# Kernel tuning notes

Hardware: AMD Instinct MI355X
Metric: run time of the kernel (lower is better)

## Reference

```python
import jax, jax.numpy as jnp
import numpy as np

H = 512  # hidden_size
L = 2    # num_layers


def setup_inputs() -> dict:
    key = jax.random.key(0)
    ks = jax.random.split(key, 10)
    B, S, I = 64, 512, 512
    s = 1.0 / np.sqrt(H)
    def w(k, shape):
        return jax.random.uniform(k, shape, jnp.float32, -s, s)
    return {
        "x": jax.random.normal(ks[0], (B, S, I), jnp.float32),
        "encoder_h": jax.random.normal(ks[1], (B, 2 * H), jnp.float32),
        "Wih_f": w(ks[2], (L, 3 * H, I)),
        "Whh_f": w(ks[3], (L, 3 * H, H)),
        "bih_f": w(ks[4], (L, 3 * H)),
        "bhh_f": w(ks[5], (L, 3 * H)),
        "Wih_b": w(ks[6], (L, 3 * H, I)),
        "Whh_b": w(ks[7], (L, 3 * H, H)),
        "bih_b": w(ks[8], (L, 3 * H)),
        "bhh_b": w(ks[9], (L, 3 * H)),
    }


def _run_direction(seq, h0, Wih, Whh, bih, bhh):
    """Stacked GRU over time. seq: [B,S,I], h0: [B,H]. Returns ([B,S,H], [B,H]).
    Equivalent to the per-timestep stacked-layer loop in the torch module: each
    layer consumes the previous layer's output stream and its own previous hidden."""
    h_last = h0
    for j in range(L):
        # Precompute input-side gates for the whole sequence (one big GEMM).
        gi = jnp.einsum('bsi,gi->bsg', seq, Wih[j]) + bih[j]  # [B,S,3H]
        Whh_j, bhh_j = Whh[j], bhh[j]

        def step(h, gi_t):
            gh = h @ Whh_j.T + bhh_j                 # [B,3H]
            i_r, i_z, i_n = jnp.split(gi_t, 3, axis=-1)
            h_r, h_z, h_n = jnp.split(gh, 3, axis=-1)
            r = jax.nn.sigmoid(i_r + h_r)
            z = jax.nn.sigmoid(i_z + h_z)
            n = jnp.tanh(i_n + r * h_n)
            h_new = (1.0 - z) * n + z * h
            return h_new, h_new

        h_last, outs = jax.lax.scan(step, h0, jnp.swapaxes(gi, 0, 1))  # outs: [S,B,H]
        seq = jnp.swapaxes(outs, 0, 1)  # [B,S,H] feeds next layer
    return seq, h_last


def reference(x, encoder_h, Wih_f, Whh_f, bih_f, bhh_f, Wih_b, Whh_b, bih_b, bhh_b):
    h0_f = encoder_h[:, :H]
    h0_b = encoder_h[:, H:]
    out_f, h_f = _run_direction(x, h0_f, Wih_f, Whh_f, bih_f, bhh_f)
    x_rev = jnp.flip(x, axis=1)
    out_b_rev, h_b = _run_direction(x_rev, h0_b, Wih_b, Whh_b, bih_b, bhh_b)
    out_b = jnp.flip(out_b_rev, axis=1)
    out = jnp.concatenate([out_f, out_b], axis=2)   # [B,S,2H]
    h = jnp.concatenate([h_f, h_b], axis=1)         # [B,2H]
    return out, h
```

## Files before the change

### kernel.cpp

```cpp
#include <hip/hip_runtime.h>


#define B_ 64
#define S_ 512
#define H_ 512
#define G3_ 1536

typedef __attribute__((ext_vector_type(8))) __bf16 bf16x8;
typedef __attribute__((ext_vector_type(8))) short short8;
typedef __attribute__((ext_vector_type(2))) unsigned long long ull2;
typedef __attribute__((ext_vector_type(4))) float f32x4;
typedef unsigned long long ull;

__device__ __forceinline__ unsigned short f2b(float f) {
  union { float f; unsigned int i; } v; v.f = f;
  unsigned int x = v.i;
  return (unsigned short)((x + 0x7fffu + ((x >> 16) & 1u)) >> 16);
}
__device__ __forceinline__ bf16x8 load8(const unsigned short* p) {
  short8 s = *(const short8*)p;
  return __builtin_bit_cast(bf16x8, s);
}
__device__ __forceinline__ bf16x8 load8f(const float* p) {
  f32x4 a = *(const f32x4*)p, b = *(const f32x4*)(p + 4);
  short8 s;
  s[0] = (short)f2b(a[0]); s[1] = (short)f2b(a[1]);
  s[2] = (short)f2b(a[2]); s[3] = (short)f2b(a[3]);
  s[4] = (short)f2b(b[0]); s[5] = (short)f2b(b[1]);
  s[6] = (short)f2b(b[2]); s[7] = (short)f2b(b[3]);
  return __builtin_bit_cast(bf16x8, s);
}
__device__ __forceinline__ f32x4 mfma16(bf16x8 a, bf16x8 b, f32x4 c) {
  return __builtin_amdgcn_mfma_f32_16x16x32_bf16(a, b, c, 0, 0, 0);
}
__device__ __forceinline__ float sigmoidf_(float x) {
  float e = __expf(-fabsf(x));
  float s = e / (1.0f + e);
  return x >= 0.0f ? 1.0f - s : s;
}
__device__ __forceinline__ float tanhf_(float x) {
  float e = __expf(-2.0f * fabsf(x));
  float r = (1.0f - e) / (1.0f + e);
  return x >= 0.0f ? r : -r;
}
__device__ __forceinline__ bf16x8 load16p(const ull* p) {
  ull2 v = *(const ull2*)p;
  return __builtin_bit_cast(bf16x8, v);
}
__device__ __forceinline__ bf16x8 ld16bypass(const ull* p) {
  short8 r;
  asm volatile("global_load_dwordx4 %0, %1, off sc0 sc1"
               : "=v"(r) : "v"(p) : "memory");
  return __builtin_bit_cast(bf16x8, r);
}

__global__ void cvt_x(const float* __restrict__ x, ull* __restrict__ xc) {
  int i = blockIdx.x * 256 + threadIdx.x;
  int b = i & 63, cell = (i >> 6) & 63, txx = i >> 12;
  const float* src = x + ((size_t)b * 512 + txx) * 512 + cell * 8;
  ull v0 = 0, v1 = 0;
#pragma unroll
  for (int j = 0; j < 4; ++j) v0 |= (ull)f2b(src[j]) << (16 * j);
#pragma unroll
  for (int j = 0; j < 4; ++j) v1 |= (ull)f2b(src[4 + j]) << (16 * j);
  size_t o = ((size_t)txx * 4096 + cell * 64 + b) * 2;
  xc[o] = v0;
  xc[o + 1] = v1;
}

__global__ void init_ring(const float* __restrict__ enc, ull* __restrict__ ring) {
  int i = blockIdx.x * 256 + threadIdx.x;
  if (i >= 32768) return;
  int gid = i >> 12;
  int u = i & 4095;
  int d = (gid >> 1) & 1, beta = gid & 1;
  int half = u & 1, b = (u >> 1) & 31, cell = u >> 6;
  const float* e = enc + (size_t)(beta * 32 + b) * 1024 + d * 512 + cell * 8 + half * 4;
  ull v = 0;
#pragma unroll
  for (int j = 0; j < 4; ++j) v |= (ull)f2b(e[j]) << (16 * j);
  ring[(size_t)gid * 32768 + 7 * 4096 + u] = v;
}

__global__ __launch_bounds__(128) void gru_fused(
    const float* __restrict__ x,
    const ull* __restrict__ xc, int usexc,
    const float* __restrict__ enc,
    const float* __restrict__ WihF, const float* __restrict__ WihB,
    const float* __restrict__ WhhF, const float* __restrict__ WhhB,
    const float* __restrict__ bihF, const float* __restrict__ bihB,
    const float* __restrict__ bhhF, const float* __restrict__ bhhB,
    ull* __restrict__ ring,
    unsigned int* __restrict__ flags,
    float* __restrict__ dout) {
  __shared__ __align__(16) unsigned short wih2[24576];
  __shared__ __align__(16) unsigned short whh2[24576];
  __shared__ float hpub[32 * 20];
  __shared__ __align__(16) float douts[8][32][20];
  __shared__ int lcnt[8];

  const int tid = threadIdx.x;
  const int lane = tid & 63;
  const int wv = tid >> 6;
  const int wg = (int)blockIdx.x;
  const int l = wg >> 7, d = (wg >> 6) & 1, beta = (wg >> 5) & 1, cb = wg & 31;
  const int gid = ((l * 2 + d) << 1) | beta;
  const int gidA = gid & 3;
  const int gidB = gidA | 4;
  const int colbase = cb * 16;
  const int rowA = lane & 15, kb = lane >> 4;

  const float* Wih = (d ? WihB : WihF) + (size_t)l * G3_ * H_;
  const float* Whh = (d ? WhhB : WhhF) + (size_t)l * G3_ * H_;
  const float* bi = (d ? bihB : bihF) + l * G3_;
  const float* bh = (d ? bhhB : bhhF) + l * G3_;

  if (tid < 8) lcnt[tid] = 0;
  for (int i = tid; i < 3072; i += 128) {
    int gate = i >> 10;
    int rest = i & 1023;
    int kk = rest >> 6;
    int l6 = rest & 63;
    int c = l6 & 15, k = l6 >> 4;
    size_t gro = (size_t)(gate * 512 + colbase + c) * 512 + kk * 32 + k * 8;
    *(short8*)&wih2[i * 8] = __builtin_bit_cast(short8, load8f(Wih + gro));
    *(short8*)&whh2[i * 8] = __builtin_bit_cast(short8, load8f(Whh + gro));
  }
  __syncthreads();

  const int col16 = rowA;
  const int hc = colbase + col16;
  const float brz_r = bi[hc] + bh[hc];
  const float brz_z = bi[512 + hc] + bh[512 + hc];
  const float bi_n = bi[1024 + hc];
  const float bh_n = bh[1024 + hc];

  const int bq = wv * 16 + kb * 4;
  const int arow = wv * 16 + rowA;

  float hm[4];
#pragma unroll
  for (int rg = 0; rg < 4; ++rg)
    hm[rg] = enc[(size_t)(beta * 32 + bq + rg) * 1024 + d * 512 + hc];

  unsigned int* flA = flags + gidA * 1024;
  unsigned int* flB = flags + gidB * 1024;
  unsigned int* flo = flags + gid * 1024;
  ull* ringA = ring + (size_t)gidA * 32768;
  ull* ringl = ring + (size_t)gid * 32768;

  const int pb = tid >> 2;
  const int pq = tid & 3;
  const int pcellL = pq >> 1, phalf = pq & 1;
  const int pidx = ((2 * cb + pcellL) * 32 + pb) * 2 + phalf;
  const int pc0 = pcellL * 8 + phalf * 4;

  for (int t = 0; t < 512; ++t) {
    bf16x8 aIn[16];
    if (l == 0) {
      int txx = d ? (511 - t) : t;
      if (usexc) {
        const ull* xp = xc + (size_t)txx * 8192;
#pragma unroll
        for (int kk = 0; kk < 16; ++kk)
          aIn[kk] = load16p(xp + (size_t)((kk * 4 + kb) * 64 + beta * 32 + arow) * 2);
      } else {
        const float* ap = x + ((size_t)(beta * 32 + arow) * 512 + txx) * 512 + kb * 8;
#pragma unroll
        for (int kk = 0; kk < 16; ++kk) aIn[kk] = load8f(ap + kk * 32);
      }
    }

    {
      const int needA = (l == 0) ? t : (t + 1);
      const int needB = (l == 0) ? (t - 7) : t;
      unsigned int* watch;
      int need;
      if (lane < 32) { watch = flA + lane * 32;        need = needA; }
      else           { watch = flB + (lane - 32) * 32; need = needB; }
      if (need > 0) {
        while (__hip_atomic_load(watch, __ATOMIC_RELAXED,
                                 __HIP_MEMORY_SCOPE_AGENT) < (unsigned)need) {}
      }
    }
    asm volatile("" ::: "memory");

    bf16x8 aOwn[16];
    ull* rpo = ringl + (size_t)((t + 7) & 7) * 4096;
#pragma unroll
    for (int kk = 0; kk < 16; ++kk)
      aOwn[kk] = ld16bypass(rpo + (size_t)((kk * 4 + kb) * 32 + arow) * 2);
    if (l == 1) {
      ull* rp = ringA + (size_t)(t & 7) * 4096;
#pragma unroll
      for (int kk = 0; kk < 16; ++kk)
        aIn[kk] = ld16bypass(rp + (size_t)((kk * 4 + kb) * 32 + arow) * 2);
    }
    asm volatile("s_waitcnt vmcnt(0)" ::: "memory");
    __builtin_amdgcn_sched_barrier(0);

    f32x4 accr = {0,0,0,0}, accz = {0,0,0,0}, acni = {0,0,0,0}, acnh = {0,0,0,0};
#pragma unroll
    for (int kk = 0; kk < 16; ++kk) {
      const int o = kk * 512 + lane * 8;
      accr = mfma16(aIn[kk],  load8(&wih2[o]), accr);
      accr = mfma16(aOwn[kk], load8(&whh2[o]), accr);
      accz = mfma16(aIn[kk],  load8(&wih2[8192 + o]), accz);
      accz = mfma16(aOwn[kk], load8(&whh2[8192 + o]), accz);
      acni = mfma16(aIn[kk],  load8(&wih2[16384 + o]), acni);
      acnh = mfma16(aOwn[kk], load8(&whh2[16384 + o]), acnh);
    }

#pragma unroll
    for (int rg = 0; rg < 4; ++rg) {
      float r = sigmoidf_(accr[rg] + brz_r);
      float z = sigmoidf_(accz[rg] + brz_z);
      float n = tanhf_(acni[rg] + bi_n + r * (acnh[rg] + bh_n));
      float hnew = (1.0f - z) * n + z * hm[rg];
      hm[rg] = hnew;
      hpub[(bq + rg) * 20 + col16] = hnew;
      if (l == 1) douts[t & 7][bq + rg][col16] = hnew;
    }
    asm volatile("" ::: "memory");

    {
      f32x4 v4 = *(f32x4*)&hpub[pb * 20 + pc0];
      ull v = 0;
      v |= (ull)f2b(v4[0]);
      v |= (ull)f2b(v4[1]) << 16;
      v |= (ull)f2b(v4[2]) << 32;
      v |= (ull)f2b(v4[3]) << 48;
      __hip_atomic_store(ringl + (size_t)(t & 7) * 4096 + pidx, v,
                         __ATOMIC_RELAXED, __HIP_MEMORY_SCOPE_AGENT);
    }
    asm volatile("s_waitcnt vmcnt(0)" ::: "memory");

    if (lane == 0) {
      int old = atomicAdd(&lcnt[t & 7], 1);
      if (old == 1) {
        lcnt[t & 7] = 0;
        __hip_atomic_store(flo + cb * 32, (unsigned)(t + 1),
                           __ATOMIC_RELAXED, __HIP_MEMORY_SCOPE_AGENT);
      }
    }

    if (l == 1 && (t & 7) == 7) {
      const int fb = tid >> 2;
      const int fc = (tid & 3) * 4;
#pragma unroll
      for (int ts = 0; ts < 8; ++ts) {
        int tt = t - 7 + ts;
        int tox = d ? (511 - tt) : tt;
        f32x4 v = *(f32x4*)&douts[ts][fb][fc];
        *(f32x4*)&dout[((size_t)(beta * 32 + fb) * 512 + tox) * 1024 +
                       d * 512 + colbase + fc] = v;
      }
    }
  }
}

__global__ void h_epi(float* __restrict__ dout) {
  int i = blockIdx.x * 256 + threadIdx.x;
  if (i >= B_ * 2 * H_) return;
  int b = i >> 10, j = i & 1023;
  int t = (j < H_) ? (S_ - 1) : 0;
  dout[(size_t)B_ * S_ * 2 * H_ + i] = dout[((size_t)b * S_ + t) * (2 * H_) + j];
}

extern "C" void kernel_launch(void* const* d_in, const int* in_sizes, int n_in,
                              void* d_out, int out_size, void* d_ws, size_t ws_size,
                              hipStream_t stream) {
  const float* x    = (const float*)d_in[0];
  const float* enc  = (const float*)d_in[1];
  const float* WihF = (const float*)d_in[2];
  const float* WhhF = (const float*)d_in[3];
  const float* bihF = (const float*)d_in[4];
  const float* bhhF = (const float*)d_in[5];
  const float* WihB = (const float*)d_in[6];
  const float* WhhB = (const float*)d_in[7];
  const float* bihB = (const float*)d_in[8];
  const float* bhhB = (const float*)d_in[9];
  float* out = (float*)d_out;

  char* ws = (char*)d_ws;
  unsigned int* flags = (unsigned int*)ws;
  ull* ring  = (ull*)(ws + 65536);
  ull* xc    = (ull*)(ws + 65536 + 2097152);
  const int usexc = (ws_size >= (size_t)65536 + 2097152 + 33554432) ? 1 : 0;

  (void)hipMemsetAsync(flags, 0, 32768, stream);
  if (usexc) cvt_x<<<8192, 256, 0, stream>>>(x, xc);
  init_ring<<<128, 256, 0, stream>>>(enc, ring);
  gru_fused<<<256, 128, 0, stream>>>(x, xc, usexc, enc,
                                     WihF, WihB, WhhF, WhhB,
                                     bihF, bihB, bhhF, bhhB,
                                     ring, flags, out);
  h_epi<<<256, 256, 0, stream>>>(out);
}
```

Before: 2.442 ms.

## Process both batch halves per workgroup, halving grid and interleaving steps

Each workgroup now handles both 32-row batch halves, looping over them inside each timestep, so the grid drops from 256 to 128 blocks. LDS-resident weights are shared across the two halves, and the work on one half can overlap the wait on the other half's flags. Ring loads switch from inline-asm cache-bypass loads to relaxed agent-scope atomic loads, and the explicit wait and sched barrier before the MFMAs are removed. The cost is serialized per-block work and half the CUs in use, which lengthens the per-step critical path.

```diff
diff --git a/kernel.cpp b/kernel.cpp
--- a/kernel.cpp
+++ b/kernel.cpp
@@ -43,15 +43,15 @@
   float r = (1.0f - e) / (1.0f + e);
   return x >= 0.0f ? r : -r;
 }
+__device__ __forceinline__ bf16x8 load16a(ull* p) {
+  ull2 v;
+  v[0] = __hip_atomic_load(p, __ATOMIC_RELAXED, __HIP_MEMORY_SCOPE_AGENT);
+  v[1] = __hip_atomic_load(p + 1, __ATOMIC_RELAXED, __HIP_MEMORY_SCOPE_AGENT);
+  return __builtin_bit_cast(bf16x8, v);
+}
 __device__ __forceinline__ bf16x8 load16p(const ull* p) {
   ull2 v = *(const ull2*)p;
   return __builtin_bit_cast(bf16x8, v);
-}
-__device__ __forceinline__ bf16x8 ld16bypass(const ull* p) {
-  short8 r;
-  asm volatile("global_load_dwordx4 %0, %1, off sc0 sc1"
-               : "=v"(r) : "v"(p) : "memory");
-  return __builtin_bit_cast(bf16x8, r);
 }
 
 __global__ void cvt_x(const float* __restrict__ x, ull* __restrict__ xc) {
@@ -95,18 +95,15 @@
     float* __restrict__ dout) {
   __shared__ __align__(16) unsigned short wih2[24576];
   __shared__ __align__(16) unsigned short whh2[24576];
-  __shared__ float hpub[32 * 20];
-  __shared__ __align__(16) float douts[8][32][20];
-  __shared__ int lcnt[8];
+  __shared__ float hpub[2][32 * 20];
+  __shared__ __align__(16) float douts[2][8][32][20];
+  __shared__ int lcnt[2][8];
 
   const int tid = threadIdx.x;
   const int lane = tid & 63;
   const int wv = tid >> 6;
   const int wg = (int)blockIdx.x;
-  const int l = wg >> 7, d = (wg >> 6) & 1, beta = (wg >> 5) & 1, cb = wg & 31;
-  const int gid = ((l * 2 + d) << 1) | beta;
-  const int gidA = gid & 3;
-  const int gidB = gidA | 4;
+  const int l = wg >> 6, d = (wg >> 5) & 1, cb = wg & 31;
   const int colbase = cb * 16;
   const int rowA = lane & 15, kb = lane >> 4;
 
@@ -115,7 +112,7 @@
   const float* bi = (d ? bihB : bihF) + l * G3_;
   const float* bh = (d ? bhhB : bhhF) + l * G3_;
 
-  if (tid < 8) lcnt[tid] = 0;
+  if (tid < 16) lcnt[tid >> 3][tid & 7] = 0;
   for (int i = tid; i < 3072; i += 128) {
     int gate = i >> 10;
     int rest = i & 1023;
@@ -138,16 +135,14 @@
   const int bq = wv * 16 + kb * 4;
   const int arow = wv * 16 + rowA;
 
-  float hm[4];
-#pragma unroll
-  for (int rg = 0; rg < 4; ++rg)
-    hm[rg] = enc[(size_t)(beta * 32 + bq + rg) * 1024 + d * 512 + hc];
-
-  unsigned int* flA = flags + gidA * 1024;
-  unsigned int* flB = flags + gidB * 1024;
-  unsigned int* flo = flags + gid * 1024;
-  ull* ringA = ring + (size_t)gidA * 32768;
-  ull* ringl = ring + (size_t)gid * 32768;
+  float hm[2][4];
+#pragma unroll
+  for (int be = 0; be < 2; ++be)
+#pragma unroll
+    for (int rg = 0; rg < 4; ++rg)
+      hm[be][rg] = enc[(size_t)(be * 32 + bq + rg) * 1024 + d * 512 + hc];
+
+  const int gidbase = (l * 2 + d) << 1;
 
   const int pb = tid >> 2;
   const int pq = tid & 3;
@@ -156,104 +151,112 @@
   const int pc0 = pcellL * 8 + phalf * 4;
 
   for (int t = 0; t < 512; ++t) {
-    bf16x8 aIn[16];
-    if (l == 0) {
-      int txx = d ? (511 - t) : t;
-      if (usexc) {
-        const ull* xp = xc + (size_t)txx * 8192;
+#pragma unroll
+    for (int be = 0; be < 2; ++be) {
+      const int gid = gidbase | be;
+      unsigned int* flA = flags + (gid & 3) * 1024;
+      unsigned int* flB = flags + ((gid & 3) | 4) * 1024;
+      unsigned int* flo = flags + gid * 1024;
+      ull* ringA = ring + (size_t)(gid & 3) * 32768;
+      ull* ringl = ring + (size_t)gid * 32768;
+
+      bf16x8 aIn[16];
+      if (l == 0) {
+        int txx = d ? (511 - t) : t;
+        if (usexc) {
+          const ull* xp = xc + (size_t)txx * 8192;
+#pragma unroll
+          for (int kk = 0; kk < 16; ++kk)
+            aIn[kk] = load16p(xp + (size_t)((kk * 4 + kb) * 64 + be * 32 + arow) * 2);
+        } else {
+          const float* ap = x + ((size_t)(be * 32 + arow) * 512 + txx) * 512 + kb * 8;
+#pragma unroll
+          for (int kk = 0; kk < 16; ++kk) aIn[kk] = load8f(ap + kk * 32);
+        }
+      }
+
+      {
+        const int needA = (l == 0) ? t : (t + 1);
+        const int needB = (l == 0) ? (t - 7) : t;
+        unsigned int* watch;
+        int need;
+        if (lane < 32) { watch = flA + lane * 32;        need = needA; }
+        else           { watch = flB + (lane - 32) * 32; need = needB; }
+        if (need > 0) {
+          while (__hip_atomic_load(watch, __ATOMIC_RELAXED,
+                                   __HIP_MEMORY_SCOPE_AGENT) < (unsigned)need) {}
+        }
+      }
+      asm volatile("" ::: "memory");
+
+      bf16x8 aOwn[16];
+      ull* rpo = ringl + (size_t)((t + 7) & 7) * 4096;
+#pragma unroll
+      for (int kk = 0; kk < 16; ++kk)
+        aOwn[kk] = load16a(rpo + (size_t)((kk * 4 + kb) * 32 + arow) * 2);
+      if (l == 1) {
+        ull* rp = ringA + (size_t)(t & 7) * 4096;
 #pragma unroll
         for (int kk = 0; kk < 16; ++kk)
-          aIn[kk] = load16p(xp + (size_t)((kk * 4 + kb) * 64 + beta * 32 + arow) * 2);
-      } else {
-        const float* ap = x + ((size_t)(beta * 32 + arow) * 512 + txx) * 512 + kb * 8;
-#pragma unroll
-        for (int kk = 0; kk < 16; ++kk) aIn[kk] = load8f(ap + kk * 32);
-      }
-    }
-
-    {
-      const int needA = (l == 0) ? t : (t + 1);
-      const int needB = (l == 0) ? (t - 7) : t;
-      unsigned int* watch;
-      int need;
-      if (lane < 32) { watch = flA + lane * 32;        need = needA; }
-      else           { watch = flB + (lane - 32) * 32; need = needB; }
-      if (need > 0) {
-        while (__hip_atomic_load(watch, __ATOMIC_RELAXED,
-                                 __HIP_MEMORY_SCOPE_AGENT) < (unsigned)need) {}
-      }
-    }
-    asm volatile("" ::: "memory");
-
-    bf16x8 aOwn[16];
-    ull* rpo = ringl + (size_t)((t + 7) & 7) * 4096;
-#pragma unroll
-    for (int kk = 0; kk < 16; ++kk)
-      aOwn[kk] = ld16bypass(rpo + (size_t)((kk * 4 + kb) * 32 + arow) * 2);
-    if (l == 1) {
-      ull* rp = ringA + (size_t)(t & 7) * 4096;
-#pragma unroll
-      for (int kk = 0; kk < 16; ++kk)
-        aIn[kk] = ld16bypass(rp + (size_t)((kk * 4 + kb) * 32 + arow) * 2);
-    }
-    asm volatile("s_waitcnt vmcnt(0)" ::: "memory");
-    __builtin_amdgcn_sched_barrier(0);
-
-    f32x4 accr = {0,0,0,0}, accz = {0,0,0,0}, acni = {0,0,0,0}, acnh = {0,0,0,0};
-#pragma unroll
-    for (int kk = 0; kk < 16; ++kk) {
-      const int o = kk * 512 + lane * 8;
-      accr = mfma16(aIn[kk],  load8(&wih2[o]), accr);
-      accr = mfma16(aOwn[kk], load8(&whh2[o]), accr);
-      accz = mfma16(aIn[kk],  load8(&wih2[8192 + o]), accz);
-      accz = mfma16(aOwn[kk], load8(&whh2[8192 + o]), accz);
-      acni = mfma16(aIn[kk],  load8(&wih2[16384 + o]), acni);
-      acnh = mfma16(aOwn[kk], load8(&whh2[16384 + o]), acnh);
-    }
-
-#pragma unroll
-    for (int rg = 0; rg < 4; ++rg) {
-      float r = sigmoidf_(accr[rg] + brz_r);
-      float z = sigmoidf_(accz[rg] + brz_z);
-      float n = tanhf_(acni[rg] + bi_n + r * (acnh[rg] + bh_n));
-      float hnew = (1.0f - z) * n + z * hm[rg];
-      hm[rg] = hnew;
-      hpub[(bq + rg) * 20 + col16] = hnew;
-      if (l == 1) douts[t & 7][bq + rg][col16] = hnew;
-    }
-    asm volatile("" ::: "memory");
-
-    {
-      f32x4 v4 = *(f32x4*)&hpub[pb * 20 + pc0];
-      ull v = 0;
-      v |= (ull)f2b(v4[0]);
-      v |= (ull)f2b(v4[1]) << 16;
-      v |= (ull)f2b(v4[2]) << 32;
-      v |= (ull)f2b(v4[3]) << 48;
-      __hip_atomic_store(ringl + (size_t)(t & 7) * 4096 + pidx, v,
-                         __ATOMIC_RELAXED, __HIP_MEMORY_SCOPE_AGENT);
-    }
-    asm volatile("s_waitcnt vmcnt(0)" ::: "memory");
-
-    if (lane == 0) {
-      int old = atomicAdd(&lcnt[t & 7], 1);
-      if (old == 1) {
-        lcnt[t & 7] = 0;
-        __hip_atomic_store(flo + cb * 32, (unsigned)(t + 1),
+          aIn[kk] = load16a(rp + (size_t)((kk * 4 + kb) * 32 + arow) * 2);
+      }
+
+      f32x4 accr = {0,0,0,0}, accz = {0,0,0,0}, acni = {0,0,0,0}, acnh = {0,0,0,0};
+#pragma unroll
+      for (int kk = 0; kk < 16; ++kk) {
+        const int o = kk * 512 + lane * 8;
+        accr = mfma16(aIn[kk],  load8(&wih2[o]), accr);
+        accr = mfma16(aOwn[kk], load8(&whh2[o]), accr);
+        accz = mfma16(aIn[kk],  load8(&wih2[8192 + o]), accz);
+        accz = mfma16(aOwn[kk], load8(&whh2[8192 + o]), accz);
+        acni = mfma16(aIn[kk],  load8(&wih2[16384 + o]), acni);
+        acnh = mfma16(aOwn[kk], load8(&whh2[16384 + o]), acnh);
+      }
+
+#pragma unroll
+      for (int rg = 0; rg < 4; ++rg) {
+        float r = sigmoidf_(accr[rg] + brz_r);
+        float z = sigmoidf_(accz[rg] + brz_z);
+        float n = tanhf_(acni[rg] + bi_n + r * (acnh[rg] + bh_n));
+        float hnew = (1.0f - z) * n + z * hm[be][rg];
+        hm[be][rg] = hnew;
+        hpub[be][(bq + rg) * 20 + col16] = hnew;
+        if (l == 1) douts[be][t & 7][bq + rg][col16] = hnew;
+      }
+      asm volatile("" ::: "memory");
+
+      {
+        f32x4 v4 = *(f32x4*)&hpub[be][pb * 20 + pc0];
+        ull v = 0;
+        v |= (ull)f2b(v4[0]);
+        v |= (ull)f2b(v4[1]) << 16;
+        v |= (ull)f2b(v4[2]) << 32;
+        v |= (ull)f2b(v4[3]) << 48;
+        __hip_atomic_store(ringl + (size_t)(t & 7) * 4096 + pidx, v,
                            __ATOMIC_RELAXED, __HIP_MEMORY_SCOPE_AGENT);
       }
-    }
-
-    if (l == 1 && (t & 7) == 7) {
-      const int fb = tid >> 2;
-      const int fc = (tid & 3) * 4;
-#pragma unroll
-      for (int ts = 0; ts < 8; ++ts) {
-        int tt = t - 7 + ts;
-        int tox = d ? (511 - tt) : tt;
-        f32x4 v = *(f32x4*)&douts[ts][fb][fc];
-        *(f32x4*)&dout[((size_t)(beta * 32 + fb) * 512 + tox) * 1024 +
-                       d * 512 + colbase + fc] = v;
+      asm volatile("s_waitcnt vmcnt(0)" ::: "memory");
+
+      if (lane == 0) {
+        int old = atomicAdd(&lcnt[be][t & 7], 1);
+        if (old == 1) {
+          lcnt[be][t & 7] = 0;
+          __hip_atomic_store(flo + cb * 32, (unsigned)(t + 1),
+                             __ATOMIC_RELAXED, __HIP_MEMORY_SCOPE_AGENT);
+        }
+      }
+
+      if (l == 1 && (t & 7) == 7) {
+        const int fb = tid >> 2;
+        const int fc = (tid & 3) * 4;
+#pragma unroll
+        for (int ts = 0; ts < 8; ++ts) {
+          int tt = t - 7 + ts;
+          int tox = d ? (511 - tt) : tt;
+          f32x4 v = *(f32x4*)&douts[be][ts][fb][fc];
+          *(f32x4*)&dout[((size_t)(be * 32 + fb) * 512 + tox) * 1024 +
+                         d * 512 + colbase + fc] = v;
+        }
       }
     }
   }
@@ -291,7 +294,7 @@
   (void)hipMemsetAsync(flags, 0, 32768, stream);
   if (usexc) cvt_x<<<8192, 256, 0, stream>>>(x, xc);
   init_ring<<<128, 256, 0, stream>>>(enc, ring);
-  gru_fused<<<256, 128, 0, stream>>>(x, xc, usexc, enc,
+  gru_fused<<<128, 128, 0, stream>>>(x, xc, usexc, enc,
                                      WihF, WihB, WhhF, WhhB,
                                      bihF, bihB, bhhF, bhhB,
                                      ring, flags, out);
```

After: 4.045 ms. +65.7%, slower.
